# Kernel tuning notes

Measured on AMD Instinct MI355X. Metric: run time of the kernel, lower is better.

## Reference

```python
import jax, jax.numpy as jnp
import numpy as np

HIDDEN = 2048
NUM_HEADS = 16
Q_LORA = 1536
KV_LORA = 512
QK_NOPE = 128
QK_ROPE = 64
V_HEAD = 128
EPS = 1e-6
QK_HEAD = QK_NOPE + QK_ROPE  # 192


def rmsnorm(x, w, eps=EPS):
    xf = x.astype(jnp.float32)
    var = jnp.mean(xf * xf, axis=-1, keepdims=True)
    return (w * (xf * jax.lax.rsqrt(var + eps)).astype(x.dtype))


def setup_inputs() -> dict:
    key = jax.random.key(0)
    ks = jax.random.split(key, 8)
    B, S = 1, 2048
    hidden_states = jax.random.normal(ks[0], (B, S, HIDDEN), dtype=jnp.float32)
    # causal additive mask [B,1,S,S]
    causal = jnp.tril(jnp.ones((S, S), dtype=bool))
    attention_mask = jnp.where(causal, 0.0, -1e9).astype(jnp.float32)[None, None]
    s = lambda fan_in: 1.0 / np.sqrt(fan_in)
    Wqa = jax.random.normal(ks[1], (HIDDEN, Q_LORA), dtype=jnp.float32) * s(HIDDEN)
    gqa = jnp.ones((Q_LORA,), dtype=jnp.float32)
    Wqb = jax.random.normal(ks[2], (Q_LORA, NUM_HEADS * QK_HEAD), dtype=jnp.float32) * s(Q_LORA)
    Wkva = jax.random.normal(ks[3], (HIDDEN, KV_LORA + QK_ROPE), dtype=jnp.float32) * s(HIDDEN)
    gkva = jnp.ones((KV_LORA,), dtype=jnp.float32)
    Wkvb = jax.random.normal(ks[4], (KV_LORA, NUM_HEADS * (QK_NOPE + V_HEAD)), dtype=jnp.float32) * s(KV_LORA)
    Wo = jax.random.normal(ks[5], (NUM_HEADS * V_HEAD, HIDDEN), dtype=jnp.float32) * s(NUM_HEADS * V_HEAD)
    return {"hidden_states": hidden_states, "attention_mask": attention_mask,
            "Wqa": Wqa, "gqa": gqa, "Wqb": Wqb, "Wkva": Wkva, "gkva": gkva,
            "Wkvb": Wkvb, "Wo": Wo}


def reference(hidden_states, attention_mask, Wqa, gqa, Wqb, Wkva, gkva, Wkvb, Wo):
    B, S, _ = hidden_states.shape
    # Q path: low-rank down-proj + RMSNorm + up-proj
    q_c = rmsnorm(hidden_states @ Wqa, gqa)
    q = (q_c @ Wqb).reshape(B, S, NUM_HEADS, QK_HEAD).transpose(0, 2, 1, 3)  # [B,H,S,192]
    # KV path: joint down-proj, split latent and shared rope part
    kv_c = hidden_states @ Wkva  # [B,S,KV_LORA+ROPE]
    kv_a, k_rope = kv_c[..., :KV_LORA], kv_c[..., KV_LORA:]
    kv = (rmsnorm(kv_a, gkva) @ Wkvb).reshape(B, S, NUM_HEADS, QK_NOPE + V_HEAD)
    k_nope, v = kv[..., :QK_NOPE], kv[..., QK_NOPE:]
    # shared rope part broadcast across heads (no rotary actually applied in source)
    k_rope_b = jnp.broadcast_to(k_rope[:, :, None, :], (B, S, NUM_HEADS, QK_ROPE))
    k = jnp.concatenate([k_nope, k_rope_b], axis=-1).transpose(0, 2, 1, 3)  # [B,H,S,192]
    v = v.transpose(0, 2, 1, 3)  # [B,H,S,128]
    scale = 1.0 / np.sqrt(QK_HEAD)
    attn = jnp.einsum("bhqd,bhkd->bhqk", q, k) * scale
    attn = attn + attention_mask
    attn = jax.nn.softmax(attn.astype(jnp.float32), axis=-1).astype(v.dtype)
    out = jnp.einsum("bhqk,bhkd->bhqd", attn, v)  # [B,H,S,128]
    out = out.transpose(0, 2, 1, 3).reshape(B, S, NUM_HEADS * V_HEAD)
    return out @ Wo
```

## Files before the change

kernel.cpp:

```cpp
#include <hip/hip_runtime.h>
#include <hip/hip_bf16.h>

typedef __bf16 bf16;
typedef __bf16 bf16x8 __attribute__((ext_vector_type(8)));
typedef __bf16 bf16x4 __attribute__((ext_vector_type(4)));
typedef float f32x4 __attribute__((ext_vector_type(4)));

#define HIDDEN 2048
#define SEQ 2048
#define NH 16
#define QL 1536
#define KVL 512
#define SCALE_LOG2E 0.10411754631f

__device__ __forceinline__ void gload_lds16(const void* g, void* l) {
  typedef const __attribute__((address_space(1))) void* gp_t;
  typedef __attribute__((address_space(3))) void* lp_t;
  __builtin_amdgcn_global_load_lds((gp_t)(unsigned long long)g,
                                   (lp_t)(unsigned int)(unsigned long long)l, 16, 0, 0);
}

__device__ __forceinline__ float fexp2(float x) {
  float r; asm("v_exp_f32 %0, %1" : "=v"(r) : "v"(x)); return r;
}

__global__ void k_prep(const float* __restrict__ hidden, bf16* __restrict__ Xb,
                       const float* __restrict__ Wqa, bf16* __restrict__ WqaT,
                       const float* __restrict__ Wqb, bf16* __restrict__ WqbT,
                       const float* __restrict__ Wkva, bf16* __restrict__ WkvaT,
                       const float* __restrict__ Wkvb, bf16* __restrict__ WkvbT,
                       const float* __restrict__ Wo, bf16* __restrict__ WoT) {
  __shared__ float tile[32][33];
  int b = blockIdx.x, tid = threadIdx.x;
  const float* W; bf16* Wt; int K, N, bx, by;
  if (b < 3072)       { W = Wqa;  Wt = WqaT;  K = 2048; N = 1536; int r = b;         bx = r % 48;  by = r / 48; }
  else if (b < 7680)  { W = Wqb;  Wt = WqbT;  K = 1536; N = 3072; int r = b - 3072;  bx = r % 96;  by = r / 96; }
  else if (b < 8832)  { W = Wkva; Wt = WkvaT; K = 2048; N = 576;  int r = b - 7680;  bx = r % 18;  by = r / 18; }
  else if (b < 10880) { W = Wkvb; Wt = WkvbT; K = 512;  N = 4096; int r = b - 8832;  bx = r % 128; by = r / 128; }
  else if (b < 14976) { W = Wo;   Wt = WoT;   K = 2048; N = 2048; int r = b - 10880; bx = r % 64;  by = r / 64; }
  else {
    int r = b - 14976;
    int base = (r * 256 + tid) * 4;
    float4 v = *(const float4*)(hidden + base);
    bf16x4 o = { (bf16)v.x, (bf16)v.y, (bf16)v.z, (bf16)v.w };
    *(bf16x4*)(Xb + base) = o;
    return;
  }
  int n0 = bx * 32, k0 = by * 32, cc = tid & 31, rr = tid >> 5;
#pragma unroll
  for (int it = 0; it < 4; ++it) {
    int r = it * 8 + rr;
    tile[r][cc] = W[(size_t)(k0 + r) * N + n0 + cc];
  }
  __syncthreads();
#pragma unroll
  for (int it = 0; it < 4; ++it) {
    int r = it * 8 + rr;
    Wt[(size_t)(n0 + r) * K + k0 + cc] = (bf16)tile[cc][r];
  }
}

__device__ __forceinline__ void gemm_body(const bf16* __restrict__ A, const bf16* __restrict__ Bt,
                                          bf16* __restrict__ Cb, float* __restrict__ Cf,
                                          int N, int K, int m0, int n0, bf16* As, bf16* Bs) {
  int tid = threadIdx.x, lane = tid & 63, w = tid >> 6;
  int wr = w >> 1, wc = w & 1;
  int l15 = lane & 15, l4 = lane >> 4;
  f32x4 acc[4][4] = {};
  for (int k0 = 0; k0 < K; k0 += 64) {
#pragma unroll
    for (int i = 0; i < 4; ++i) {
      int c = w * 4 + i;
      int row = c * 8 + (lane >> 3);
      int col = (lane & 7) * 8;
      gload_lds16(&A[(size_t)(m0 + row) * K + k0 + col], &As[c * 512]);
      gload_lds16(&Bt[(size_t)(n0 + row) * K + k0 + col], &Bs[c * 512]);
    }
    __syncthreads();
#pragma unroll
    for (int kk = 0; kk < 2; ++kk) {
      bf16x8 af[4], bfr[4];
#pragma unroll
      for (int m = 0; m < 4; ++m)
        af[m] = *(const bf16x8*)&As[(wr * 64 + m * 16 + l15) * 64 + kk * 32 + l4 * 8];
#pragma unroll
      for (int n = 0; n < 4; ++n)
        bfr[n] = *(const bf16x8*)&Bs[(wc * 64 + n * 16 + l15) * 64 + kk * 32 + l4 * 8];
      __builtin_amdgcn_s_setprio(1);
#pragma unroll
      for (int m = 0; m < 4; ++m)
#pragma unroll
        for (int n = 0; n < 4; ++n)
          acc[m][n] = __builtin_amdgcn_mfma_f32_16x16x32_bf16(af[m], bfr[n], acc[m][n], 0, 0, 0);
      __builtin_amdgcn_s_setprio(0);
    }
    __syncthreads();
  }
#pragma unroll
  for (int m = 0; m < 4; ++m)
#pragma unroll
    for (int n = 0; n < 4; ++n)
#pragma unroll
      for (int r = 0; r < 4; ++r) {
        int grow = m0 + wr * 64 + m * 16 + l4 * 4 + r;
        int gcol = n0 + wc * 64 + n * 16 + l15;
        if (gcol < N) {
          float v = acc[m][n][r];
          if (Cf) Cf[(size_t)grow * N + gcol] = v;
          else Cb[(size_t)grow * N + gcol] = (bf16)v;
        }
      }
}

__global__ __launch_bounds__(256) void k_gemm(const bf16* __restrict__ A, const bf16* __restrict__ Bt,
                                              bf16* __restrict__ Cb, float* __restrict__ Cf,
                                              int N, int K) {
  __shared__ __align__(16) bf16 As[128 * 64];
  __shared__ __align__(16) bf16 Bs[128 * 64];
  gemm_body(A, Bt, Cb, Cf, N, K, blockIdx.x * 128, blockIdx.y * 128, As, Bs);
}

__global__ __launch_bounds__(256) void k_gemm_a(const bf16* __restrict__ Xb,
                                                const bf16* __restrict__ B1, const bf16* __restrict__ B2,
                                                float* __restrict__ C1, float* __restrict__ C2) {
  __shared__ __align__(16) bf16 As[128 * 64];
  __shared__ __align__(16) bf16 Bs[128 * 64];
  int by = blockIdx.y;
  if (by < 12) gemm_body(Xb, B1, nullptr, C1, 1536, 2048, blockIdx.x * 128, by * 128, As, Bs);
  else         gemm_body(Xb, B2, nullptr, C2, 576, 2048, blockIdx.x * 128, (by - 12) * 128, As, Bs);
}

__global__ __launch_bounds__(256) void k_gemm_b(const bf16* __restrict__ A1, const bf16* __restrict__ A2,
                                                const bf16* __restrict__ B1, const bf16* __restrict__ B2,
                                                bf16* __restrict__ C1, bf16* __restrict__ C2) {
  __shared__ __align__(16) bf16 As[128 * 64];
  __shared__ __align__(16) bf16 Bs[128 * 64];
  int by = blockIdx.y;
  if (by < 24) gemm_body(A1, B1, C1, nullptr, 3072, 1536, blockIdx.x * 128, by * 128, As, Bs);
  else         gemm_body(A2, B2, C2, nullptr, 4096, 512, blockIdx.x * 128, (by - 24) * 128, As, Bs);
}

__device__ inline float block_reduce_sum(float v, float* red) {
#pragma unroll
  for (int off = 1; off < 64; off <<= 1) v += __shfl_xor(v, off);
  int w = threadIdx.x >> 6;
  if ((threadIdx.x & 63) == 0) red[w] = v;
  __syncthreads();
  return red[0] + red[1] + red[2] + red[3];
}

__global__ void k_rms_all(const float* __restrict__ qa, const float* __restrict__ gq, bf16* __restrict__ qc,
                          const float* __restrict__ kvc, const float* __restrict__ gkv,
                          bf16* __restrict__ kvn, bf16* __restrict__ kr) {
  __shared__ float red[4];
  int b = blockIdx.x, tid = threadIdx.x;
  if (b < 2048) {
    int row = b;
    float v[6];
    float ss = 0.f;
#pragma unroll
    for (int j = 0; j < 6; ++j) {
      v[j] = qa[(size_t)row * QL + tid + j * 256];
      ss += v[j] * v[j];
    }
    float tot = block_reduce_sum(ss, red);
    float rs = rsqrtf(tot / (float)QL + 1e-6f);
#pragma unroll
    for (int j = 0; j < 6; ++j) {
      int c = tid + j * 256;
      qc[(size_t)row * QL + c] = (bf16)(v[j] * rs * gq[c]);
    }
  } else {
    int row = b - 2048;
    float v0 = kvc[(size_t)row * 576 + tid];
    float v1 = kvc[(size_t)row * 576 + tid + 256];
    float tot = block_reduce_sum(v0 * v0 + v1 * v1, red);
    float rs = rsqrtf(tot / (float)KVL + 1e-6f);
    kvn[(size_t)row * KVL + tid] = (bf16)(v0 * rs * gkv[tid]);
    kvn[(size_t)row * KVL + tid + 256] = (bf16)(v1 * rs * gkv[tid + 256]);
    if (tid < 64) kr[row * 64 + tid] = (bf16)kvc[(size_t)row * 576 + 512 + tid];
  }
}

__global__ void k_vt(const bf16* __restrict__ KVm, bf16* __restrict__ VT) {
  __shared__ bf16 tile[32][34];
  int b = blockIdx.x, tid = threadIdx.x;
  int h = b >> 8, rem = b & 255;
  int d0 = (rem >> 6) * 32, s0 = (rem & 63) * 32;
  int cc = tid & 31, rr = tid >> 5;
#pragma unroll
  for (int it = 0; it < 4; ++it) {
    int r = it * 8 + rr;
    tile[r][cc] = KVm[(size_t)(s0 + r) * 4096 + h * 256 + 128 + d0 + cc];
  }
  __syncthreads();
#pragma unroll
  for (int it = 0; it < 4; ++it) {
    int r = it * 8 + rr;
    VT[((size_t)(h * 128 + d0 + r)) * 2048 + s0 + cc] = tile[cc][r];
  }
}

__global__ __launch_bounds__(256) void k_attn(const bf16* __restrict__ Q, const bf16* __restrict__ KV,
                                              const bf16* __restrict__ KR, const bf16* __restrict__ VT,
                                              bf16* __restrict__ O,
                                              bf16* __restrict__ Opart, float2* __restrict__ Ml) {
  __shared__ __align__(16) bf16 Ks[64 * 200];
  __shared__ __align__(16) bf16 Vt[128 * 72];
  __shared__ __align__(16) bf16 Ps[4 * 16 * 72];
  int bid = blockIdx.x;
  int h = bid & 15, cid = bid >> 4;
  int qb, ch, nc;
  if (cid < 8)       { qb = cid; ch = 0; nc = 1; }
  else if (cid < 24) { int r = cid - 8;  qb = 8 + (r >> 1); ch = r & 1; nc = 2; }
  else if (cid < 48) { int r = cid - 24; qb = 16 + r / 3;   ch = r % 3; nc = 3; }
  else               { int r = cid - 48; qb = 24 + (r >> 2); ch = r & 3; nc = 4; }
  int t0 = ch * 8;
  int t1 = t0 + 8 < qb + 1 ? t0 + 8 : qb + 1;
  int q0 = qb * 64;
  int tid = threadIdx.x, lane = tid & 63, w = tid >> 6;
  int l15 = lane & 15, l4 = lane >> 4;
  bf16* Pw = Ps + w * 16 * 72;
  const bf16* VTh = VT + (size_t)h * 128 * 2048;

  bf16x8 aq[6];
  int qrow = q0 + w * 16 + l15;
#pragma unroll
  for (int ks = 0; ks < 6; ++ks)
    aq[ks] = *(const bf16x8*)&Q[(size_t)qrow * 3072 + h * 192 + ks * 32 + l4 * 8];

  bf16x8 ones_b;
  {
    float ov = (l15 == 0) ? 1.0f : 0.0f;
#pragma unroll
    for (int j = 0; j < 8; ++j) ones_b[j] = (bf16)ov;
  }

  f32x4 oacc[8] = {};
  f32x4 o9 = {0.f, 0.f, 0.f, 0.f};
  float m[4] = {-1e30f, -1e30f, -1e30f, -1e30f};
  for (int t = t0; t < t1; ++t) {
#pragma unroll
    for (int it = 0; it < 6; ++it) {
      int idx = it * 256 + tid;
      int r = idx / 24, gg = idx % 24;
      int p = t * 64 + r;
      int4 val;
      if (gg < 16) val = *(const int4*)&KV[(size_t)p * 4096 + h * 256 + gg * 8];
      else         val = *(const int4*)&KR[(size_t)p * 64 + (gg - 16) * 8];
      *(int4*)&Ks[r * 200 + gg * 8] = val;
    }
#pragma unroll
    for (int it = 0; it < 4; ++it) {
      int idx = it * 256 + tid;
      int d = idx >> 3, c = idx & 7;
      *(int4*)&Vt[d * 72 + c * 8] = *(const int4*)&VTh[(size_t)d * 2048 + t * 64 + c * 8];
    }
    __syncthreads();

    f32x4 sacc[4] = {};
    __builtin_amdgcn_s_setprio(1);
#pragma unroll
    for (int ks = 0; ks < 6; ++ks)
#pragma unroll
      for (int n = 0; n < 4; ++n) {
        bf16x8 bk = *(const bf16x8*)&Ks[(n * 16 + l15) * 200 + ks * 32 + l4 * 8];
        sacc[n] = __builtin_amdgcn_mfma_f32_16x16x32_bf16(aq[ks], bk, sacc[n], 0, 0, 0);
      }
    __builtin_amdgcn_s_setprio(0);

    bool lastt = (t == qb);
#pragma unroll
    for (int n = 0; n < 4; ++n)
#pragma unroll
      for (int r = 0; r < 4; ++r) {
        float v = sacc[n][r] * SCALE_LOG2E;
        if (lastt) {
          int col = t * 64 + n * 16 + l15;
          int rowg = q0 + w * 16 + l4 * 4 + r;
          if (col > rowg) v = -1e30f;
        }
        sacc[n][r] = v;
      }

    float pmax[4];
#pragma unroll
    for (int r = 0; r < 4; ++r) {
      float mx = fmaxf(fmaxf(sacc[0][r], sacc[1][r]), fmaxf(sacc[2][r], sacc[3][r]));
      mx = fmaxf(mx, __shfl_xor(mx, 1));
      mx = fmaxf(mx, __shfl_xor(mx, 2));
      mx = fmaxf(mx, __shfl_xor(mx, 4));
      mx = fmaxf(mx, __shfl_xor(mx, 8));
      pmax[r] = mx;
    }
    float need = 0.f;
#pragma unroll
    for (int r = 0; r < 4; ++r) need = fmaxf(need, pmax[r] - m[r]);
    if (__any(need > 8.0f)) {
#pragma unroll
      for (int r = 0; r < 4; ++r) {
        float mn = fmaxf(m[r], pmax[r]);
        float al = fexp2(m[r] - mn);
        m[r] = mn;
#pragma unroll
        for (int vf = 0; vf < 8; ++vf) oacc[vf][r] *= al;
        o9[r] *= al;
      }
    }

#pragma unroll
    for (int n = 0; n < 4; ++n)
#pragma unroll
      for (int r = 0; r < 4; ++r)
        Pw[(l4 * 4 + r) * 72 + n * 16 + l15] = (bf16)fexp2(sacc[n][r] - m[r]);

    __builtin_amdgcn_s_setprio(1);
#pragma unroll
    for (int ks = 0; ks < 2; ++ks) {
      bf16x8 ap = *(const bf16x8*)&Pw[l15 * 72 + ks * 32 + l4 * 8];
      o9 = __builtin_amdgcn_mfma_f32_16x16x32_bf16(ap, ones_b, o9, 0, 0, 0);
#pragma unroll
      for (int vf = 0; vf < 8; ++vf) {
        bf16x8 bv = *(const bf16x8*)&Vt[(vf * 16 + l15) * 72 + ks * 32 + l4 * 8];
        oacc[vf] = __builtin_amdgcn_mfma_f32_16x16x32_bf16(ap, bv, oacc[vf], 0, 0, 0);
      }
    }
    __builtin_amdgcn_s_setprio(0);
    __syncthreads();
  }

  if (nc == 1) {
#pragma unroll
    for (int r = 0; r < 4; ++r) {
      float ls = __shfl(o9[r], lane & 48);
      float inv = 1.0f / ls;
#pragma unroll
      for (int vf = 0; vf < 8; ++vf) {
        int rowg = q0 + w * 16 + l4 * 4 + r;
        int col = h * 128 + vf * 16 + l15;
        O[(size_t)rowg * 2048 + col] = (bf16)(oacc[vf][r] * inv);
      }
    }
  } else {
    bf16* Op = Opart + (size_t)bid * 64 * 128;
#pragma unroll
    for (int r = 0; r < 4; ++r) {
      int row = w * 16 + l4 * 4 + r;
#pragma unroll
      for (int vf = 0; vf < 8; ++vf)
        Op[row * 128 + vf * 16 + l15] = (bf16)oacc[vf][r];
      if (l15 == 0) Ml[bid * 64 + row] = make_float2(m[r], o9[r]);
    }
  }
}

__global__ __launch_bounds__(256) void k_comb(const bf16* __restrict__ Opart,
                                              const float2* __restrict__ Ml,
                                              bf16* __restrict__ O) {
  int b = blockIdx.x, h = b & 15, qb = 8 + (b >> 4);
  int cid0, nc;
  if (qb < 16)      { cid0 = 8 + 2 * (qb - 8);   nc = 2; }
  else if (qb < 24) { cid0 = 24 + 3 * (qb - 16); nc = 3; }
  else              { cid0 = 48 + 4 * (qb - 24); nc = 4; }
  int tid = threadIdx.x;
  int rr = tid >> 5, col = (tid & 31) * 4;
  int slot0 = cid0 * 16 + h;
#pragma unroll
  for (int rp = 0; rp < 8; ++rp) {
    int row = rp * 8 + rr;
    float M = -1e30f;
    for (int c = 0; c < nc; ++c) M = fmaxf(M, Ml[(slot0 + c * 16) * 64 + row].x);
    float acc0 = 0.f, acc1 = 0.f, acc2 = 0.f, acc3 = 0.f, L = 0.f;
    for (int c = 0; c < nc; ++c) {
      int slot = slot0 + c * 16;
      float2 ml = Ml[slot * 64 + row];
      float wgt = fexp2(ml.x - M);
      L += wgt * ml.y;
      bf16x4 v = *(const bf16x4*)&Opart[(size_t)slot * 64 * 128 + row * 128 + col];
      acc0 += wgt * (float)v[0];
      acc1 += wgt * (float)v[1];
      acc2 += wgt * (float)v[2];
      acc3 += wgt * (float)v[3];
    }
    float inv = 1.0f / L;
    bf16x4 o = { (bf16)(acc0 * inv), (bf16)(acc1 * inv), (bf16)(acc2 * inv), (bf16)(acc3 * inv) };
    *(bf16x4*)&O[(size_t)(qb * 64 + row) * 2048 + h * 128 + col] = o;
  }
}

extern "C" void kernel_launch(void* const* d_in, const int* in_sizes, int n_in,
                              void* d_out, int out_size, void* d_ws, size_t ws_size,
                              hipStream_t stream) {
  (void)in_sizes; (void)n_in; (void)out_size; (void)ws_size;
  const float* hidden = (const float*)d_in[0];
  const float* Wqa  = (const float*)d_in[2];
  const float* gqa  = (const float*)d_in[3];
  const float* Wqb  = (const float*)d_in[4];
  const float* Wkva = (const float*)d_in[5];
  const float* gkva = (const float*)d_in[6];
  const float* Wkvb = (const float*)d_in[7];
  const float* Wo   = (const float*)d_in[8];
  float* out = (float*)d_out;

  char* ws = (char*)d_ws;
  size_t off = 0;
  auto alloc = [&](size_t bytes) {
    char* p = ws + off;
    off += (bytes + 255) & ~(size_t)255;
    return p;
  };
  bf16* Xb     = (bf16*)alloc((size_t)SEQ * HIDDEN * 2);
  bf16* WqaT   = (bf16*)alloc((size_t)QL * HIDDEN * 2);
  bf16* WqbT   = (bf16*)alloc((size_t)3072 * QL * 2);
  bf16* WkvaT  = (bf16*)alloc((size_t)576 * HIDDEN * 2);
  bf16* WkvbT  = (bf16*)alloc((size_t)4096 * KVL * 2);
  bf16* WoT    = (bf16*)alloc((size_t)2048 * 2048 * 2);
  float* qa    = (float*)alloc((size_t)SEQ * QL * 4);
  float* kvc   = (float*)alloc((size_t)SEQ * 576 * 4);
  bf16* qc     = (bf16*)alloc((size_t)SEQ * QL * 2);
  bf16* kvn    = (bf16*)alloc((size_t)SEQ * KVL * 2);
  bf16* krope  = (bf16*)alloc((size_t)SEQ * 64 * 2);
  bf16* Qm     = (bf16*)alloc((size_t)SEQ * 3072 * 2);
  bf16* KVm    = (bf16*)alloc((size_t)SEQ * 4096 * 2);
  bf16* VTg    = (bf16*)alloc((size_t)NH * 128 * SEQ * 2);
  bf16* Om     = (bf16*)alloc((size_t)SEQ * 2048 * 2);
  float2* Ml   = (float2*)alloc((size_t)1280 * 64 * 8);
  bf16* Opart  = (bf16*)qa;

  k_prep<<<19072, 256, 0, stream>>>(hidden, Xb, Wqa, WqaT, Wqb, WqbT,
                                    Wkva, WkvaT, Wkvb, WkvbT, Wo, WoT);
  k_gemm_a<<<dim3(16, 17), 256, 0, stream>>>(Xb, WqaT, WkvaT, qa, kvc);
  k_rms_all<<<4096, 256, 0, stream>>>(qa, gqa, qc, kvc, gkva, kvn, krope);
  k_gemm_b<<<dim3(16, 56), 256, 0, stream>>>(qc, kvn, WqbT, WkvbT, Qm, KVm);
  k_vt<<<4096, 256, 0, stream>>>(KVm, VTg);
  k_attn<<<1280, 256, 0, stream>>>(Qm, KVm, krope, VTg, Om, Opart, Ml);
  k_comb<<<384, 256, 0, stream>>>(Opart, Ml, Om);
  k_gemm<<<dim3(16, 16), 256, 0, stream>>>(Om, WoT, nullptr, out, 2048, 2048);
}
```

Before: 252.8 us.

## Use 8-wave blocks for GEMMs and 128-row query tiles in attention

The GEMMs move from 4 to 8 waves per block. Each wave now computes a 64x32 sub-tile instead of 64x64, which cuts accumulator registers per wave and raises the wave count per CU. Attention blocks now cover 128 query rows with 8 waves and share each K/V tile load across twice as many queries. The causal chunk split and the combine kernel are rewritten for 128-row blocks, and an XOR swizzle is added to the V tile in LDS to avoid bank conflicts. The cost is half as many attention blocks, coarser load balancing, and more masking work on the diagonal tiles.

```diff
diff --git a/kernel.cpp b/kernel.cpp
--- a/kernel.cpp
+++ b/kernel.cpp
@@ -64,13 +64,13 @@
                                           bf16* __restrict__ Cb, float* __restrict__ Cf,
                                           int N, int K, int m0, int n0, bf16* As, bf16* Bs) {
   int tid = threadIdx.x, lane = tid & 63, w = tid >> 6;
-  int wr = w >> 1, wc = w & 1;
+  int wr = w >> 2, wc = w & 3;
   int l15 = lane & 15, l4 = lane >> 4;
-  f32x4 acc[4][4] = {};
+  f32x4 acc[4][2] = {};
   for (int k0 = 0; k0 < K; k0 += 64) {
 #pragma unroll
-    for (int i = 0; i < 4; ++i) {
-      int c = w * 4 + i;
+    for (int i = 0; i < 2; ++i) {
+      int c = w * 2 + i;
       int row = c * 8 + (lane >> 3);
       int col = (lane & 7) * 8;
       gload_lds16(&A[(size_t)(m0 + row) * K + k0 + col], &As[c * 512]);
@@ -79,18 +79,18 @@
     __syncthreads();
 #pragma unroll
     for (int kk = 0; kk < 2; ++kk) {
-      bf16x8 af[4], bfr[4];
+      bf16x8 af[4], bfr[2];
 #pragma unroll
       for (int m = 0; m < 4; ++m)
         af[m] = *(const bf16x8*)&As[(wr * 64 + m * 16 + l15) * 64 + kk * 32 + l4 * 8];
 #pragma unroll
-      for (int n = 0; n < 4; ++n)
-        bfr[n] = *(const bf16x8*)&Bs[(wc * 64 + n * 16 + l15) * 64 + kk * 32 + l4 * 8];
+      for (int n = 0; n < 2; ++n)
+        bfr[n] = *(const bf16x8*)&Bs[(wc * 32 + n * 16 + l15) * 64 + kk * 32 + l4 * 8];
       __builtin_amdgcn_s_setprio(1);
 #pragma unroll
       for (int m = 0; m < 4; ++m)
 #pragma unroll
-        for (int n = 0; n < 4; ++n)
+        for (int n = 0; n < 2; ++n)
           acc[m][n] = __builtin_amdgcn_mfma_f32_16x16x32_bf16(af[m], bfr[n], acc[m][n], 0, 0, 0);
       __builtin_amdgcn_s_setprio(0);
     }
@@ -99,11 +99,11 @@
 #pragma unroll
   for (int m = 0; m < 4; ++m)
 #pragma unroll
-    for (int n = 0; n < 4; ++n)
+    for (int n = 0; n < 2; ++n)
 #pragma unroll
       for (int r = 0; r < 4; ++r) {
         int grow = m0 + wr * 64 + m * 16 + l4 * 4 + r;
-        int gcol = n0 + wc * 64 + n * 16 + l15;
+        int gcol = n0 + wc * 32 + n * 16 + l15;
         if (gcol < N) {
           float v = acc[m][n][r];
           if (Cf) Cf[(size_t)grow * N + gcol] = v;
@@ -112,7 +112,7 @@
       }
 }
 
-__global__ __launch_bounds__(256) void k_gemm(const bf16* __restrict__ A, const bf16* __restrict__ Bt,
+__global__ __launch_bounds__(512) void k_gemm(const bf16* __restrict__ A, const bf16* __restrict__ Bt,
                                               bf16* __restrict__ Cb, float* __restrict__ Cf,
                                               int N, int K) {
   __shared__ __align__(16) bf16 As[128 * 64];
@@ -120,7 +120,7 @@
   gemm_body(A, Bt, Cb, Cf, N, K, blockIdx.x * 128, blockIdx.y * 128, As, Bs);
 }
 
-__global__ __launch_bounds__(256) void k_gemm_a(const bf16* __restrict__ Xb,
+__global__ __launch_bounds__(512) void k_gemm_a(const bf16* __restrict__ Xb,
                                                 const bf16* __restrict__ B1, const bf16* __restrict__ B2,
                                                 float* __restrict__ C1, float* __restrict__ C2) {
   __shared__ __align__(16) bf16 As[128 * 64];
@@ -130,7 +130,7 @@
   else         gemm_body(Xb, B2, nullptr, C2, 576, 2048, blockIdx.x * 128, (by - 12) * 128, As, Bs);
 }
 
-__global__ __launch_bounds__(256) void k_gemm_b(const bf16* __restrict__ A1, const bf16* __restrict__ A2,
+__global__ __launch_bounds__(512) void k_gemm_b(const bf16* __restrict__ A1, const bf16* __restrict__ A2,
                                                 const bf16* __restrict__ B1, const bf16* __restrict__ B2,
                                                 bf16* __restrict__ C1, bf16* __restrict__ C2) {
   __shared__ __align__(16) bf16 As[128 * 64];
@@ -201,23 +201,23 @@
   }
 }
 
-__global__ __launch_bounds__(256) void k_attn(const bf16* __restrict__ Q, const bf16* __restrict__ KV,
+__global__ __launch_bounds__(512) void k_attn(const bf16* __restrict__ Q, const bf16* __restrict__ KV,
                                               const bf16* __restrict__ KR, const bf16* __restrict__ VT,
                                               bf16* __restrict__ O,
                                               bf16* __restrict__ Opart, float2* __restrict__ Ml) {
   __shared__ __align__(16) bf16 Ks[64 * 200];
   __shared__ __align__(16) bf16 Vt[128 * 72];
-  __shared__ __align__(16) bf16 Ps[4 * 16 * 72];
+  __shared__ __align__(16) bf16 Ps[8 * 16 * 72];
   int bid = blockIdx.x;
   int h = bid & 15, cid = bid >> 4;
-  int qb, ch, nc;
-  if (cid < 8)       { qb = cid; ch = 0; nc = 1; }
-  else if (cid < 24) { int r = cid - 8;  qb = 8 + (r >> 1); ch = r & 1; nc = 2; }
-  else if (cid < 48) { int r = cid - 24; qb = 16 + r / 3;   ch = r % 3; nc = 3; }
-  else               { int r = cid - 48; qb = 24 + (r >> 2); ch = r & 3; nc = 4; }
-  int t0 = ch * 8;
-  int t1 = t0 + 8 < qb + 1 ? t0 + 8 : qb + 1;
-  int q0 = qb * 64;
+  int qbp, ch, nc;
+  if (cid < 4)       { qbp = cid; ch = 0; nc = 1; }
+  else if (cid < 12) { int r = cid - 4;  qbp = 4 + (r >> 1);  ch = r & 1; nc = 2; }
+  else if (cid < 24) { int r = cid - 12; qbp = 8 + r / 3;     ch = r % 3; nc = 3; }
+  else               { int r = cid - 24; qbp = 12 + (r >> 2); ch = r & 3; nc = 4; }
+  int T = 2 * qbp + 2;
+  int t0 = ch * T / nc, t1 = (ch + 1) * T / nc;
+  int q0 = qbp * 128;
   int tid = threadIdx.x, lane = tid & 63, w = tid >> 6;
   int l15 = lane & 15, l4 = lane >> 4;
   bf16* Pw = Ps + w * 16 * 72;
@@ -241,8 +241,8 @@
   float m[4] = {-1e30f, -1e30f, -1e30f, -1e30f};
   for (int t = t0; t < t1; ++t) {
 #pragma unroll
-    for (int it = 0; it < 6; ++it) {
-      int idx = it * 256 + tid;
+    for (int it = 0; it < 3; ++it) {
+      int idx = it * 512 + tid;
       int r = idx / 24, gg = idx % 24;
       int p = t * 64 + r;
       int4 val;
@@ -251,10 +251,11 @@
       *(int4*)&Ks[r * 200 + gg * 8] = val;
     }
 #pragma unroll
-    for (int it = 0; it < 4; ++it) {
-      int idx = it * 256 + tid;
+    for (int it = 0; it < 2; ++it) {
+      int idx = it * 512 + tid;
       int d = idx >> 3, c = idx & 7;
-      *(int4*)&Vt[d * 72 + c * 8] = *(const int4*)&VTh[(size_t)d * 2048 + t * 64 + c * 8];
+      *(int4*)&Vt[d * 72 + ((c ^ (d & 7)) * 8)] =
+          *(const int4*)&VTh[(size_t)d * 2048 + t * 64 + c * 8];
     }
     __syncthreads();
 
@@ -269,13 +270,13 @@
       }
     __builtin_amdgcn_s_setprio(0);
 
-    bool lastt = (t == qb);
+    bool maskt = (t >= 2 * qbp);
 #pragma unroll
     for (int n = 0; n < 4; ++n)
 #pragma unroll
       for (int r = 0; r < 4; ++r) {
         float v = sacc[n][r] * SCALE_LOG2E;
-        if (lastt) {
+        if (maskt) {
           int col = t * 64 + n * 16 + l15;
           int rowg = q0 + w * 16 + l4 * 4 + r;
           if (col > rowg) v = -1e30f;
@@ -321,7 +322,8 @@
       o9 = __builtin_amdgcn_mfma_f32_16x16x32_bf16(ap, ones_b, o9, 0, 0, 0);
 #pragma unroll
       for (int vf = 0; vf < 8; ++vf) {
-        bf16x8 bv = *(const bf16x8*)&Vt[(vf * 16 + l15) * 72 + ks * 32 + l4 * 8];
+        int dd = vf * 16 + l15;
+        bf16x8 bv = *(const bf16x8*)&Vt[dd * 72 + (((ks * 4 + l4) ^ (dd & 7)) * 8)];
         oacc[vf] = __builtin_amdgcn_mfma_f32_16x16x32_bf16(ap, bv, oacc[vf], 0, 0, 0);
       }
     }
@@ -342,14 +344,14 @@
       }
     }
   } else {
-    bf16* Op = Opart + (size_t)bid * 64 * 128;
+    bf16* Op = Opart + (size_t)bid * 128 * 128;
 #pragma unroll
     for (int r = 0; r < 4; ++r) {
       int row = w * 16 + l4 * 4 + r;
 #pragma unroll
       for (int vf = 0; vf < 8; ++vf)
         Op[row * 128 + vf * 16 + l15] = (bf16)oacc[vf][r];
-      if (l15 == 0) Ml[bid * 64 + row] = make_float2(m[r], o9[r]);
+      if (l15 == 0) Ml[bid * 128 + row] = make_float2(m[r], o9[r]);
     }
   }
 }
@@ -357,26 +359,25 @@
 __global__ __launch_bounds__(256) void k_comb(const bf16* __restrict__ Opart,
                                               const float2* __restrict__ Ml,
                                               bf16* __restrict__ O) {
-  int b = blockIdx.x, h = b & 15, qb = 8 + (b >> 4);
+  int b = blockIdx.x, h = b & 15, qbp = 4 + (b >> 4);
   int cid0, nc;
-  if (qb < 16)      { cid0 = 8 + 2 * (qb - 8);   nc = 2; }
-  else if (qb < 24) { cid0 = 24 + 3 * (qb - 16); nc = 3; }
-  else              { cid0 = 48 + 4 * (qb - 24); nc = 4; }
+  if (qbp < 8)       { cid0 = 4 + 2 * (qbp - 4);   nc = 2; }
+  else if (qbp < 12) { cid0 = 12 + 3 * (qbp - 8);  nc = 3; }
+  else               { cid0 = 24 + 4 * (qbp - 12); nc = 4; }
   int tid = threadIdx.x;
   int rr = tid >> 5, col = (tid & 31) * 4;
-  int slot0 = cid0 * 16 + h;
-#pragma unroll
-  for (int rp = 0; rp < 8; ++rp) {
+#pragma unroll
+  for (int rp = 0; rp < 16; ++rp) {
     int row = rp * 8 + rr;
     float M = -1e30f;
-    for (int c = 0; c < nc; ++c) M = fmaxf(M, Ml[(slot0 + c * 16) * 64 + row].x);
+    for (int c = 0; c < nc; ++c) M = fmaxf(M, Ml[((cid0 + c) * 16 + h) * 128 + row].x);
     float acc0 = 0.f, acc1 = 0.f, acc2 = 0.f, acc3 = 0.f, L = 0.f;
     for (int c = 0; c < nc; ++c) {
-      int slot = slot0 + c * 16;
-      float2 ml = Ml[slot * 64 + row];
+      int slot = (cid0 + c) * 16 + h;
+      float2 ml = Ml[slot * 128 + row];
       float wgt = fexp2(ml.x - M);
       L += wgt * ml.y;
-      bf16x4 v = *(const bf16x4*)&Opart[(size_t)slot * 64 * 128 + row * 128 + col];
+      bf16x4 v = *(const bf16x4*)&Opart[(size_t)slot * 128 * 128 + row * 128 + col];
       acc0 += wgt * (float)v[0];
       acc1 += wgt * (float)v[1];
       acc2 += wgt * (float)v[2];
@@ -384,7 +385,7 @@
     }
     float inv = 1.0f / L;
     bf16x4 o = { (bf16)(acc0 * inv), (bf16)(acc1 * inv), (bf16)(acc2 * inv), (bf16)(acc3 * inv) };
-    *(bf16x4*)&O[(size_t)(qb * 64 + row) * 2048 + h * 128 + col] = o;
+    *(bf16x4*)&O[(size_t)(qbp * 128 + row) * 2048 + h * 128 + col] = o;
   }
 }
 
@@ -424,16 +425,16 @@
   bf16* KVm    = (bf16*)alloc((size_t)SEQ * 4096 * 2);
   bf16* VTg    = (bf16*)alloc((size_t)NH * 128 * SEQ * 2);
   bf16* Om     = (bf16*)alloc((size_t)SEQ * 2048 * 2);
-  float2* Ml   = (float2*)alloc((size_t)1280 * 64 * 8);
+  float2* Ml   = (float2*)alloc((size_t)640 * 128 * 8);
   bf16* Opart  = (bf16*)qa;
 
   k_prep<<<19072, 256, 0, stream>>>(hidden, Xb, Wqa, WqaT, Wqb, WqbT,
                                     Wkva, WkvaT, Wkvb, WkvbT, Wo, WoT);
-  k_gemm_a<<<dim3(16, 17), 256, 0, stream>>>(Xb, WqaT, WkvaT, qa, kvc);
+  k_gemm_a<<<dim3(16, 17), 512, 0, stream>>>(Xb, WqaT, WkvaT, qa, kvc);
   k_rms_all<<<4096, 256, 0, stream>>>(qa, gqa, qc, kvc, gkva, kvn, krope);
-  k_gemm_b<<<dim3(16, 56), 256, 0, stream>>>(qc, kvn, WqbT, WkvbT, Qm, KVm);
+  k_gemm_b<<<dim3(16, 56), 512, 0, stream>>>(qc, kvn, WqbT, WkvbT, Qm, KVm);
   k_vt<<<4096, 256, 0, stream>>>(KVm, VTg);
-  k_attn<<<1280, 256, 0, stream>>>(Qm, KVm, krope, VTg, Om, Opart, Ml);
-  k_comb<<<384, 256, 0, stream>>>(Opart, Ml, Om);
-  k_gemm<<<dim3(16, 16), 256, 0, stream>>>(Om, WoT, nullptr, out, 2048, 2048);
-}
+  k_attn<<<640, 512, 0, stream>>>(Qm, KVm, krope, VTg, Om, Opart, Ml);
+  k_comb<<<192, 256, 0, stream>>>(Opart, Ml, Om);
+  k_gemm<<<dim3(16, 16), 512, 0, stream>>>(Om, WoT, nullptr, out, 2048, 2048);
+}
```

After: 280.5 us. +11.0%, slower.
